# Kernel tuning notes

Measured on AMD Instinct MI355X. Metric: run time of the kernel, lower is better.

The kernel has to match this reference:

```python
import jax, jax.numpy as jnp
import numpy as np

B, C, H, W = 8, 128, 48, 48
RED = 16  # SELayer reduction


def setup_inputs() -> dict:
    key = jax.random.key(0)
    ks = jax.random.split(key, 8)
    s = 0.05  # weight scale for numerical stability of softmax
    return {
        "x": jax.random.normal(ks[0], (B, C, H, W), jnp.float32),
        "Wq": jax.random.normal(ks[1], (C, C), jnp.float32) * s,
        "bq": jnp.zeros((C,), jnp.float32),
        "Wk": jax.random.normal(ks[2], (C, C), jnp.float32) * s,
        "bk": jnp.zeros((C,), jnp.float32),
        "Wv": jax.random.normal(ks[3], (C, C), jnp.float32) * s,
        "bv": jnp.zeros((C,), jnp.float32),
        "se_w1": jax.random.normal(ks[4], (C // RED, C), jnp.float32) * s,
        "se_w2": jax.random.normal(ks[5], (C, C // RED), jnp.float32) * s,
        "gamma": jax.random.normal(ks[6], (1,), jnp.float32),
    }


def reference(x, Wq, bq, Wk, bk, Wv, bv, se_w1, se_w2, gamma):
    b, c, h, w = x.shape
    n = h * w
    xf = x.reshape(b, c, n)  # (B, C, N)
    # 1x1 convs == per-pixel linear maps over channels
    q = jnp.einsum('oc,bcn->bon', Wq, xf) + bq[None, :, None]  # (B, C, N)
    k = jnp.einsum('oc,bcn->bon', Wk, xf) + bk[None, :, None]
    v = jnp.einsum('oc,bcn->bon', Wv, xf) + bv[None, :, None]
    # energy[b, i, j] = sum_c q[b, c, i] * k[b, c, j]  (unscaled, as in source)
    energy = jnp.einsum('bci,bcj->bij', q, k)  # (B, N, N)
    attn = jax.nn.softmax(energy, axis=-1)
    # out[b, c, i] = sum_j v[b, c, j] * attn[b, i, j]
    out = jnp.einsum('bcj,bij->bci', v, attn).reshape(b, c, h, w)
    # SELayer applied to the input x
    y = jnp.mean(x, axis=(2, 3))  # (B, C) global average pool
    y = jax.nn.relu(y @ se_w1.T)  # (B, C//RED)
    y = jax.nn.sigmoid(y @ se_w2.T)  # (B, C)
    x_se = x * y[:, :, None, None]
    return gamma[0] * out + x_se
```

## Files before the change

kernel.cpp:

```cpp
#include <hip/hip_runtime.h>

typedef _Float16 half8 __attribute__((ext_vector_type(8)));
typedef _Float16 half4 __attribute__((ext_vector_type(4)));
typedef float f32x4 __attribute__((ext_vector_type(4)));

#define BATCH 8
#define CH 128
#define NPIX 2304
#define SPLIT 4
#define JPER (NPIX / SPLIT)
#define BN (BATCH * NPIX)
#define LOG2E 1.44269504088896f

__device__ __forceinline__ f32x4 mfma32(half8 a, half8 b, f32x4 c) {
    return __builtin_amdgcn_mfma_f32_16x16x32_f16(a, b, c, 0, 0, 0);
}
__device__ __forceinline__ f32x4 mfma16(half4 a, half4 b, f32x4 c) {
    return __builtin_amdgcn_mfma_f32_16x16x16f16(a, b, c, 0, 0, 0);
}

__device__ __forceinline__ void gl_lds16(const _Float16* g, _Float16* l) {
    typedef const __attribute__((address_space(1))) unsigned int gu32;
    typedef __attribute__((address_space(3))) unsigned int lu32;
    __builtin_amdgcn_global_load_lds((gu32*)g, (lu32*)l, 16, 0, 0);
}

__global__ __launch_bounds__(256) void k_prep(
        const float* __restrict__ x, const float* __restrict__ Wq,
        const float* __restrict__ Wk, const float* __restrict__ Wv,
        _Float16* __restrict__ Wh, float* __restrict__ y0) {
    const int bid = blockIdx.x;
    const int t = threadIdx.x;
    if (bid < 1024) {
        const int row = bid;
        const float4* p = (const float4*)(x + (size_t)row * NPIX);
        float s = 0.f;
        for (int tt = t; tt < NPIX / 4; tt += 256) {
            float4 v = p[tt];
            s += v.x + v.y + v.z + v.w;
        }
        for (int m = 1; m < 64; m <<= 1) s += __shfl_xor(s, m);
        __shared__ float ls[4];
        if ((t & 63) == 0) ls[t >> 6] = s;
        __syncthreads();
        if (t == 0) y0[row] = (ls[0] + ls[1] + ls[2] + ls[3]) * (1.0f / (float)NPIX);
    } else {
        int i = (bid - 1024) * 256 + t;
        const float* src = (i < 16384) ? Wq : ((i < 32768) ? Wk : Wv);
        Wh[i] = (_Float16)src[i & 16383];
    }
}

__global__ __launch_bounds__(256) void k_proj(
        const float* __restrict__ x, const _Float16* __restrict__ Wh,
        const float* __restrict__ bq, const float* __restrict__ bk, const float* __restrict__ bv,
        _Float16* __restrict__ qT, _Float16* __restrict__ kT, _Float16* __restrict__ vN,
        const float* __restrict__ y0, const float* __restrict__ se_w1,
        const float* __restrict__ se_w2, float* __restrict__ scale) {
    const int which = blockIdx.z;
    const int t = threadIdx.x;

    if (which == 3) {
        if (blockIdx.x != 0 || blockIdx.y != 0) return;
        __shared__ float ly[128];
        __shared__ float ly1[8];
        for (int b = 0; b < BATCH; ++b) {
            if (t < 128) ly[t] = y0[b * 128 + t];
            __syncthreads();
            if (t < 8) {
                float a = 0.f;
                for (int c = 0; c < 128; ++c) a += se_w1[t * 128 + c] * ly[c];
                ly1[t] = fmaxf(a, 0.f);
            }
            __syncthreads();
            if (t < 128) {
                float a = 0.f;
                for (int r = 0; r < 8; ++r) a += se_w2[t * 8 + r] * ly1[r];
                scale[b * 128 + t] = 1.f / (1.f + __expf(-a));
            }
            __syncthreads();
        }
        return;
    }

    const int n0 = blockIdx.x * 128;
    const int b = blockIdx.y;
    const float* bias = (which == 0) ? bq : ((which == 1) ? bk : bv);
    const _Float16* W = Wh + which * 16384;

    __shared__ __align__(16) _Float16 xt[128 * 128];

    {
        const float* xb = x + (size_t)b * CH * NPIX + n0;
        for (int rep = 0; rep < 16; ++rep) {
            int flat = rep * 256 + t;
            int c = flat >> 5;
            int n4 = (flat & 31) * 4;
            float4 v4 = *(const float4*)(xb + (size_t)c * NPIX + n4);
            int cc = c & 7, ck = c >> 3;
            xt[(n4 + 0) * 128 + ((ck ^ ((n4 + 0) & 7)) * 8) + cc] = (_Float16)v4.x;
            xt[(n4 + 1) * 128 + ((ck ^ ((n4 + 1) & 7)) * 8) + cc] = (_Float16)v4.y;
            xt[(n4 + 2) * 128 + ((ck ^ ((n4 + 2) & 7)) * 8) + cc] = (_Float16)v4.z;
            xt[(n4 + 3) * 128 + ((ck ^ ((n4 + 3) & 7)) * 8) + cc] = (_Float16)v4.w;
        }
    }
    __syncthreads();

    const int lane = t & 63, w = t >> 6;
    const int ln15 = lane & 15, quad = lane >> 4;

    f32x4 zero4 = {0.f, 0.f, 0.f, 0.f};
    f32x4 acc[8][2];
    for (int mt = 0; mt < 8; ++mt) { acc[mt][0] = zero4; acc[mt][1] = zero4; }

    for (int ks = 0; ks < 4; ++ks) {
        half8 bf[2];
        for (int nt = 0; nt < 2; ++nt) {
            int row = w * 32 + nt * 16 + ln15;
            int ch = ks * 4 + quad;
            bf[nt] = *(const half8*)(xt + row * 128 + ((ch ^ (row & 7)) * 8));
        }
        for (int mt = 0; mt < 8; ++mt) {
            half8 af = *(const half8*)(W + (mt * 16 + ln15) * 128 + ks * 32 + quad * 8);
            acc[mt][0] = mfma32(af, bf[0], acc[mt][0]);
            acc[mt][1] = mfma32(af, bf[1], acc[mt][1]);
        }
    }
    __syncthreads();

    if (which == 2) {
        for (int mt = 0; mt < 8; ++mt)
            for (int nt = 0; nt < 2; ++nt)
                for (int r = 0; r < 4; ++r) {
                    int c = mt * 16 + quad * 4 + r;
                    int nl = w * 32 + nt * 16 + ln15;
                    xt[c * 128 + (((nl >> 3) ^ (c & 7)) * 8) + (nl & 7)] =
                        (_Float16)(acc[mt][nt][r] + bias[c]);
                }
        __syncthreads();
        _Float16* vb = vN + (size_t)b * CH * NPIX + n0;
        for (int rep = 0; rep < 8; ++rep) {
            int c = rep * 16 + (t >> 4), ch = t & 15;
            *(half8*)(vb + (size_t)c * NPIX + ch * 8) =
                *(const half8*)(xt + c * 128 + ((ch ^ (c & 7)) * 8));
        }
    } else {
        for (int mt = 0; mt < 8; ++mt)
            for (int nt = 0; nt < 2; ++nt)
                for (int r = 0; r < 4; ++r) {
                    int c = mt * 16 + quad * 4 + r;
                    int nl = w * 32 + nt * 16 + ln15;
                    xt[nl * 128 + (((c >> 3) ^ (nl & 7)) * 8) + (c & 7)] =
                        (_Float16)(acc[mt][nt][r] + bias[c]);
                }
        __syncthreads();
        _Float16* dst = ((which == 0) ? qT : kT) + ((size_t)b * NPIX + n0) * CH;
        for (int rep = 0; rep < 8; ++rep) {
            int nl = rep * 16 + (t >> 4), ch = t & 15;
            *(half8*)(dst + nl * 128 + ch * 8) =
                *(const half8*)(xt + nl * 128 + ((ch ^ (nl & 7)) * 8));
        }
    }
}

__global__ __launch_bounds__(256, 2) void k_attn(
        const _Float16* __restrict__ qT, const _Float16* __restrict__ kT,
        const _Float16* __restrict__ vN,
        _Float16* __restrict__ o_part, float* __restrict__ g_m, float* __restrict__ g_l) {
    const int i0 = blockIdx.x * 64;
    const int b = blockIdx.y;
    const int split = blockIdx.z;
    const int t = threadIdx.x;
    const int lane = t & 63, w = t >> 6;
    const int ln15 = lane & 15, quad = lane >> 4;

    __shared__ __align__(16) _Float16 sh[32768];

    half8 qf[4];
    {
        const _Float16* qb = qT + ((size_t)b * NPIX + i0 + w * 16 + ln15) * CH + quad * 8;
        for (int kc = 0; kc < 4; ++kc) qf[kc] = *(const half8*)(qb + kc * 32);
    }

    const _Float16* kb0 = kT + ((size_t)b * NPIX) * CH;
    const _Float16* vb0 = vN + (size_t)b * CH * NPIX;

    auto stage = [&](int j0, _Float16* buf) {
        #pragma unroll
        for (int r = 0; r < 4; ++r) {
            int idx = r * 4 + w;
            int row = 4 * idx + (lane >> 4);
            int ch  = (lane & 15) ^ (row & 7);
            gl_lds16(kb0 + (size_t)(j0 + row) * CH + ch * 8,
                     buf + idx * 512);
        }
        #pragma unroll
        for (int r = 0; r < 4; ++r) {
            int idx = r * 4 + w;
            int c  = 8 * idx + (lane >> 3);
            int ch = (lane & 7) ^ (c & 7);
            gl_lds16(vb0 + (size_t)c * NPIX + j0 + ch * 8,
                     buf + 8192 + idx * 512);
        }
    };

    stage(split * JPER, sh);
    __syncthreads();

    f32x4 zero4 = {0.f, 0.f, 0.f, 0.f};
    f32x4 os[8];
    for (int ct = 0; ct < 8; ++ct) os[ct] = zero4;
    float m = -1e30f, l = 0.f;
    int cur = 0;

    for (int it = 0; it < 9; ++it) {
        _Float16* k_s = sh + cur * 16384;
        _Float16* v_s = k_s + 8192;

        if (it < 8) stage(split * JPER + (it + 1) * 64, sh + (cur ^ 1) * 16384);

        f32x4 s[4];
        for (int jt = 0; jt < 4; ++jt) s[jt] = zero4;
        __builtin_amdgcn_s_setprio(1);
        for (int jt = 0; jt < 4; ++jt) {
            for (int kc = 0; kc < 4; ++kc) {
                int row = jt * 16 + ln15, ch = kc * 4 + quad;
                half8 kf = *(const half8*)(k_s + row * 128 + ((ch ^ (row & 7)) * 8));
                s[jt] = mfma32(kf, qf[kc], s[jt]);
            }
        }
        __builtin_amdgcn_s_setprio(0);

        float mx = fmaxf(fmaxf(s[0][0], s[0][1]), fmaxf(s[0][2], s[0][3]));
        for (int jt = 1; jt < 4; ++jt)
            mx = fmaxf(mx, fmaxf(fmaxf(s[jt][0], s[jt][1]), fmaxf(s[jt][2], s[jt][3])));
        mx = fmaxf(mx, __shfl_xor(mx, 16));
        mx = fmaxf(mx, __shfl_xor(mx, 32));
        if (!__all(mx - m <= 8.0f)) {
            float mnew = fmaxf(m, mx);
            float alpha = exp2f((m - mnew) * LOG2E);
            for (int ct = 0; ct < 8; ++ct) {
                os[ct][0] *= alpha; os[ct][1] *= alpha;
                os[ct][2] *= alpha; os[ct][3] *= alpha;
            }
            l *= alpha;
            m = mnew;
        }
        float mbias = m * LOG2E;

        float sum = 0.f;
        half4 pf[4];
        for (int jt = 0; jt < 4; ++jt)
            for (int r = 0; r < 4; ++r) {
                float p = exp2f(fmaf(s[jt][r], LOG2E, -mbias));
                sum += p;
                pf[jt][r] = (_Float16)p;
            }
        sum += __shfl_xor(sum, 16);
        sum += __shfl_xor(sum, 32);
        l += sum;

        __builtin_amdgcn_s_setprio(1);
        for (int ct = 0; ct < 8; ++ct) {
            int c = ct * 16 + ln15;
            for (int jt = 0; jt < 4; ++jt) {
                int chunk = jt * 2 + (quad >> 1);
                half4 vf = *(const half4*)(v_s + c * 64 + ((chunk ^ (c & 7)) * 8) + (quad & 1) * 4);
                os[ct] = mfma16(vf, pf[jt], os[ct]);
            }
        }
        __builtin_amdgcn_s_setprio(0);

        __syncthreads();
        cur ^= 1;
    }

    if (quad == 0) {
        int i = i0 + w * 16 + ln15;
        g_m[(size_t)(split * BATCH + b) * NPIX + i] = m;
        g_l[(size_t)(split * BATCH + b) * NPIX + i] = l;
    }
    const float linv = 1.0f / l;
    for (int ct = 0; ct < 8; ++ct)
        for (int r = 0; r < 4; ++r) {
            int c = ct * 16 + quad * 4 + r;
            int il = w * 16 + ln15;
            int chunk = (il >> 3);
            sh[c * 64 + ((chunk ^ (c & 7)) * 8) + (il & 7)] = (_Float16)(os[ct][r] * linv);
        }
    __syncthreads();
    _Float16* op = o_part + (size_t)(split * BATCH + b) * CH * NPIX;
    for (int rep = 0; rep < 4; ++rep) {
        int c = rep * 32 + (t >> 3), ch = t & 7;
        *(half8*)(op + (size_t)c * NPIX + i0 + ch * 8) =
            *(const half8*)(sh + c * 64 + ((ch ^ (c & 7)) * 8));
    }
}

__global__ __launch_bounds__(256) void k_combine(
        const _Float16* __restrict__ o_part, const float* __restrict__ g_m,
        const float* __restrict__ g_l, const float* __restrict__ x,
        const float* __restrict__ scale, const float* __restrict__ gamma_p,
        float* __restrict__ out) {
    const int i0 = blockIdx.x * 64;
    const int b = blockIdx.y;
    const int t = threadIdx.x;
    __shared__ float wl[SPLIT][64];

    if (t < 64) {
        int i = i0 + t;
        float mm[SPLIT], llv[SPLIT];
        float M = -1e30f;
        for (int s = 0; s < SPLIT; ++s) {
            mm[s] = g_m[(size_t)(s * BATCH + b) * NPIX + i];
            llv[s] = g_l[(size_t)(s * BATCH + b) * NPIX + i];
            M = fmaxf(M, mm[s]);
        }
        float L = 0.f, e[SPLIT];
        for (int s = 0; s < SPLIT; ++s) {
            e[s] = exp2f((mm[s] - M) * LOG2E);
            L += e[s] * llv[s];
        }
        float inv = 1.f / L;
        for (int s = 0; s < SPLIT; ++s) wl[s][t] = e[s] * llv[s] * inv;
    }
    __syncthreads();

    const float g = gamma_p[0];
    for (int rep = 0; rep < 4; ++rep) {
        int c = rep * 32 + (t >> 3), i8 = (t & 7) * 8;
        size_t base = ((size_t)b * CH + c) * NPIX + i0 + i8;
        float acc[8] = {0.f, 0.f, 0.f, 0.f, 0.f, 0.f, 0.f, 0.f};
        for (int s = 0; s < SPLIT; ++s) {
            half8 o = *(const half8*)(o_part +
                ((size_t)(s * BATCH + b) * CH + c) * NPIX + i0 + i8);
            for (int e = 0; e < 8; ++e) acc[e] += wl[s][i8 + e] * (float)o[e];
        }
        float sc = scale[b * 128 + c];
        float4 x0 = *(const float4*)(x + base);
        float4 x1 = *(const float4*)(x + base + 4);
        float4 r0, r1;
        r0.x = g * acc[0] + x0.x * sc; r0.y = g * acc[1] + x0.y * sc;
        r0.z = g * acc[2] + x0.z * sc; r0.w = g * acc[3] + x0.w * sc;
        r1.x = g * acc[4] + x1.x * sc; r1.y = g * acc[5] + x1.y * sc;
        r1.z = g * acc[6] + x1.z * sc; r1.w = g * acc[7] + x1.w * sc;
        *(float4*)(out + base) = r0;
        *(float4*)(out + base + 4) = r1;
    }
}

extern "C" void kernel_launch(void* const* d_in, const int* in_sizes, int n_in,
                              void* d_out, int out_size, void* d_ws, size_t ws_size,
                              hipStream_t stream) {
    const float* x     = (const float*)d_in[0];
    const float* Wq    = (const float*)d_in[1];
    const float* bq    = (const float*)d_in[2];
    const float* Wk    = (const float*)d_in[3];
    const float* bk    = (const float*)d_in[4];
    const float* Wv    = (const float*)d_in[5];
    const float* bv    = (const float*)d_in[6];
    const float* se_w1 = (const float*)d_in[7];
    const float* se_w2 = (const float*)d_in[8];
    const float* gamma = (const float*)d_in[9];
    float* out = (float*)d_out;

    char* ws = (char*)d_ws;
    const size_t E = (size_t)BATCH * NPIX * CH;
    _Float16* qT = (_Float16*)(ws);
    _Float16* kT = (_Float16*)(ws + E * 2);
    _Float16* vN = (_Float16*)(ws + E * 4);
    _Float16* op = (_Float16*)(ws + E * 6);
    char* tail   = ws + E * 6 + (size_t)SPLIT * E * 2;
    _Float16* Wh = (_Float16*)(tail);
    float* g_m   = (float*)(tail + 98304);
    float* g_l   = (float*)(tail + 98304 + SPLIT * BN * 4);
    float* y0    = (float*)(tail + 98304 + 2 * SPLIT * BN * 4);
    float* scale = (float*)(tail + 98304 + 2 * SPLIT * BN * 4 + 4096);

    k_prep<<<1216, 256, 0, stream>>>(x, Wq, Wk, Wv, Wh, y0);
    k_proj<<<dim3(NPIX / 128, BATCH, 4), 256, 0, stream>>>(
        x, Wh, bq, bk, bv, qT, kT, vN, y0, se_w1, se_w2, scale);
    k_attn<<<dim3(NPIX / 64, BATCH, SPLIT), 256, 0, stream>>>(
        qT, kT, vN, op, g_m, g_l);
    k_combine<<<dim3(NPIX / 64, BATCH), 256, 0, stream>>>(
        op, g_m, g_l, x, scale, gamma, out);
}
```

Before: 162.9 us.

## Single-buffer attention LDS, raise split and occupancy, pack half2 stores in projection

```diff
diff --git a/kernel.cpp b/kernel.cpp
--- a/kernel.cpp
+++ b/kernel.cpp
@@ -2,13 +2,15 @@
 
 typedef _Float16 half8 __attribute__((ext_vector_type(8)));
 typedef _Float16 half4 __attribute__((ext_vector_type(4)));
+typedef _Float16 half2v __attribute__((ext_vector_type(2)));
 typedef float f32x4 __attribute__((ext_vector_type(4)));
 
 #define BATCH 8
 #define CH 128
 #define NPIX 2304
-#define SPLIT 4
+#define SPLIT 6
 #define JPER (NPIX / SPLIT)
+#define NT (JPER / 64)
 #define BN (BATCH * NPIX)
 #define LOG2E 1.44269504088896f
 
@@ -92,16 +94,21 @@
 
     {
         const float* xb = x + (size_t)b * CH * NPIX + n0;
-        for (int rep = 0; rep < 16; ++rep) {
+        for (int rep = 0; rep < 8; ++rep) {
             int flat = rep * 256 + t;
-            int c = flat >> 5;
+            int c2 = (flat >> 5) * 2;
             int n4 = (flat & 31) * 4;
-            float4 v4 = *(const float4*)(xb + (size_t)c * NPIX + n4);
-            int cc = c & 7, ck = c >> 3;
-            xt[(n4 + 0) * 128 + ((ck ^ ((n4 + 0) & 7)) * 8) + cc] = (_Float16)v4.x;
-            xt[(n4 + 1) * 128 + ((ck ^ ((n4 + 1) & 7)) * 8) + cc] = (_Float16)v4.y;
-            xt[(n4 + 2) * 128 + ((ck ^ ((n4 + 2) & 7)) * 8) + cc] = (_Float16)v4.z;
-            xt[(n4 + 3) * 128 + ((ck ^ ((n4 + 3) & 7)) * 8) + cc] = (_Float16)v4.w;
+            float4 va = *(const float4*)(xb + (size_t)c2 * NPIX + n4);
+            float4 vb = *(const float4*)(xb + (size_t)(c2 + 1) * NPIX + n4);
+            int cc = c2 & 7, ck = c2 >> 3;
+            *(half2v*)(xt + (n4 + 0) * 128 + ((ck ^ ((n4 + 0) & 7)) * 8) + cc) =
+                (half2v){(_Float16)va.x, (_Float16)vb.x};
+            *(half2v*)(xt + (n4 + 1) * 128 + ((ck ^ ((n4 + 1) & 7)) * 8) + cc) =
+                (half2v){(_Float16)va.y, (_Float16)vb.y};
+            *(half2v*)(xt + (n4 + 2) * 128 + ((ck ^ ((n4 + 2) & 7)) * 8) + cc) =
+                (half2v){(_Float16)va.z, (_Float16)vb.z};
+            *(half2v*)(xt + (n4 + 3) * 128 + ((ck ^ ((n4 + 3) & 7)) * 8) + cc) =
+                (half2v){(_Float16)va.w, (_Float16)vb.w};
         }
     }
     __syncthreads();
@@ -147,11 +154,12 @@
     } else {
         for (int mt = 0; mt < 8; ++mt)
             for (int nt = 0; nt < 2; ++nt)
-                for (int r = 0; r < 4; ++r) {
+                for (int r = 0; r < 4; r += 2) {
                     int c = mt * 16 + quad * 4 + r;
                     int nl = w * 32 + nt * 16 + ln15;
-                    xt[nl * 128 + (((c >> 3) ^ (nl & 7)) * 8) + (c & 7)] =
-                        (_Float16)(acc[mt][nt][r] + bias[c]);
+                    *(half2v*)(xt + nl * 128 + (((c >> 3) ^ (nl & 7)) * 8) + (c & 7)) =
+                        (half2v){(_Float16)(acc[mt][nt][r] + bias[c]),
+                                 (_Float16)(acc[mt][nt][r + 1] + bias[c + 1])};
                 }
         __syncthreads();
         _Float16* dst = ((which == 0) ? qT : kT) + ((size_t)b * NPIX + n0) * CH;
@@ -163,7 +171,7 @@
     }
 }
 
-__global__ __launch_bounds__(256, 2) void k_attn(
+__global__ __launch_bounds__(256, 5) void k_attn(
         const _Float16* __restrict__ qT, const _Float16* __restrict__ kT,
         const _Float16* __restrict__ vN,
         _Float16* __restrict__ o_part, float* __restrict__ g_m, float* __restrict__ g_l) {
@@ -174,7 +182,9 @@
     const int lane = t & 63, w = t >> 6;
     const int ln15 = lane & 15, quad = lane >> 4;
 
-    __shared__ __align__(16) _Float16 sh[32768];
+    __shared__ __align__(16) _Float16 sh[16384];
+    _Float16* k_s = sh;
+    _Float16* v_s = sh + 8192;
 
     half8 qf[4];
     {
@@ -182,42 +192,37 @@
         for (int kc = 0; kc < 4; ++kc) qf[kc] = *(const half8*)(qb + kc * 32);
     }
 
-    const _Float16* kb0 = kT + ((size_t)b * NPIX) * CH;
-    const _Float16* vb0 = vN + (size_t)b * CH * NPIX;
-
-    auto stage = [&](int j0, _Float16* buf) {
+    const _Float16* kbase[4];
+    const _Float16* vbase[4];
+    #pragma unroll
+    for (int r = 0; r < 4; ++r) {
+        int idx = r * 4 + w;
+        int row = 4 * idx + (lane >> 4);
+        int kch = (lane & 15) ^ (row & 7);
+        kbase[r] = kT + (size_t)b * NPIX * CH + (size_t)row * CH + kch * 8;
+        int c = 8 * idx + (lane >> 3);
+        int vch = (lane & 7) ^ (c & 7);
+        vbase[r] = vN + (size_t)b * CH * NPIX + (size_t)c * NPIX + vch * 8;
+    }
+
+    auto stage = [&](int j0) {
         #pragma unroll
-        for (int r = 0; r < 4; ++r) {
-            int idx = r * 4 + w;
-            int row = 4 * idx + (lane >> 4);
-            int ch  = (lane & 15) ^ (row & 7);
-            gl_lds16(kb0 + (size_t)(j0 + row) * CH + ch * 8,
-                     buf + idx * 512);
-        }
+        for (int r = 0; r < 4; ++r)
+            gl_lds16(kbase[r] + (size_t)j0 * CH, k_s + (r * 4 + w) * 512);
         #pragma unroll
-        for (int r = 0; r < 4; ++r) {
-            int idx = r * 4 + w;
-            int c  = 8 * idx + (lane >> 3);
-            int ch = (lane & 7) ^ (c & 7);
-            gl_lds16(vb0 + (size_t)c * NPIX + j0 + ch * 8,
-                     buf + 8192 + idx * 512);
-        }
+        for (int r = 0; r < 4; ++r)
+            gl_lds16(vbase[r] + j0, v_s + (r * 4 + w) * 512);
     };
 
-    stage(split * JPER, sh);
-    __syncthreads();
+    stage(split * JPER);
 
     f32x4 zero4 = {0.f, 0.f, 0.f, 0.f};
     f32x4 os[8];
     for (int ct = 0; ct < 8; ++ct) os[ct] = zero4;
     float m = -1e30f, l = 0.f;
-    int cur = 0;
-
-    for (int it = 0; it < 9; ++it) {
-        _Float16* k_s = sh + cur * 16384;
-        _Float16* v_s = k_s + 8192;
-
-        if (it < 8) stage(split * JPER + (it + 1) * 64, sh + (cur ^ 1) * 16384);
+
+    for (int it = 0; it < NT; ++it) {
+        __syncthreads();
 
         f32x4 s[4];
         for (int jt = 0; jt < 4; ++jt) s[jt] = zero4;
@@ -271,8 +276,10 @@
         }
         __builtin_amdgcn_s_setprio(0);
 
-        __syncthreads();
-        cur ^= 1;
+        if (it < NT - 1) {
+            __syncthreads();
+            stage(split * JPER + (it + 1) * 64);
+        }
     }
 
     if (quad == 0) {
@@ -281,6 +288,7 @@
         g_l[(size_t)(split * BATCH + b) * NPIX + i] = l;
     }
     const float linv = 1.0f / l;
+    __syncthreads();
     for (int ct = 0; ct < 8; ++ct)
         for (int r = 0; r < 4; ++r) {
             int c = ct * 16 + quad * 4 + r;
@@ -373,9 +381,9 @@
     char* tail   = ws + E * 6 + (size_t)SPLIT * E * 2;
     _Float16* Wh = (_Float16*)(tail);
     float* g_m   = (float*)(tail + 98304);
-    float* g_l   = (float*)(tail + 98304 + SPLIT * BN * 4);
-    float* y0    = (float*)(tail + 98304 + 2 * SPLIT * BN * 4);
-    float* scale = (float*)(tail + 98304 + 2 * SPLIT * BN * 4 + 4096);
+    float* g_l   = (float*)(tail + 98304 + (size_t)SPLIT * BN * 4);
+    float* y0    = (float*)(tail + 98304 + 2 * (size_t)SPLIT * BN * 4);
+    float* scale = (float*)(tail + 98304 + 2 * (size_t)SPLIT * BN * 4 + 4096);
 
     k_prep<<<1216, 256, 0, stream>>>(x, Wq, Wk, Wv, Wh, y0);
     k_proj<<<dim3(NPIX / 128, BATCH, 4), 256, 0, stream>>>(
```

After: 167.8 us. 3.1% more time.
